# Optimization experiments

Hardware: AMD Instinct MI355X
Metric: run time of the kernel (lower is better)

## Reference

```python
import jax, jax.numpy as jnp
import numpy as np
from jax import lax

N, CIN, COUT, T, V, G, K = 32, 64, 64, 256, 25, 8, 3  # batch, channels, time, joints, groups, subsets
EPS = 1e-5  # BatchNorm eps


def setup_inputs() -> dict:
    key = jax.random.key(0)
    ks = jax.random.split(key, 10)
    x = jax.random.normal(ks[0], (N, CIN, T, V), jnp.float32)
    # DecoupleA param: A reshaped [3,1,V,V] tiled over groups (torch .repeat tiles)
    A0 = jax.random.uniform(ks[1], (K, 1, V, V), jnp.float32)
    DecoupleA = jnp.tile(A0, (1, G, 1, 1))
    W = jax.random.normal(ks[2], (CIN, COUT * K), jnp.float32) * np.float32(np.sqrt(0.5 / (COUT * K)))
    b = jnp.full((1, COUT * K, 1, 1), 1e-6, jnp.float32)
    g0 = 1.0 + 0.1 * jax.random.normal(ks[3], (COUT * K,), jnp.float32)
    b0 = 0.1 * jax.random.normal(ks[4], (COUT * K,), jnp.float32)
    g1 = 1.0 + 0.1 * jax.random.normal(ks[5], (COUT,), jnp.float32)
    b1 = 0.1 * jax.random.normal(ks[6], (COUT,), jnp.float32)
    conv_w = jax.random.normal(ks[7], (COUT, COUT, 9, 1), jnp.float32) * np.float32(np.sqrt(2.0 / (COUT * 9)))
    conv_b = jnp.zeros((COUT,), jnp.float32)
    g2 = 1.0 + 0.1 * jax.random.normal(ks[8], (COUT,), jnp.float32)
    b2 = 0.1 * jax.random.normal(ks[9], (COUT,), jnp.float32)
    return {"x": x, "DecoupleA": DecoupleA, "W": W, "b": b, "g0": g0, "b0": b0,
            "g1": g1, "b1": b1, "conv_w": conv_w, "conv_b": conv_b, "g2": g2, "b2": b2,
            "keep_prob": 1}


def _bn_eval(y, g, be):
    # inference BN with running_mean=0, running_var=1
    return y * (g / jnp.sqrt(1.0 + EPS))[None, :, None, None] + be[None, :, None, None]


def reference(x, DecoupleA, W, b, g0, b0, g1, b1, conv_w, conv_b, g2, b2, keep_prob):
    # ---- unit_gcn ----
    learn_A = jnp.tile(DecoupleA, (1, COUT // G, 1, 1))           # [3, COUT, V, V]
    # norm(): right-multiply by diag((colsum + 0.001)^-1) == scale columns
    invD = 1.0 / (jnp.sum(learn_A, axis=2) + 0.001)               # [3, COUT, V]
    normA = learn_A * invD[:, :, None, :]
    y = jnp.einsum('nctw,cd->ndtw', x, W) + b                     # [N, 3*COUT, T, V]
    y = _bn_eval(y, g0, b0)
    y = y.reshape(N, K, COUT, T, V)
    y = jnp.einsum('nkctv,kcvw->nctw', y, normA)                  # message passing
    y = _bn_eval(y, g1, b1)
    y = jax.nn.relu(y + x)                                        # down = identity (CIN==COUT)
    # ---- unit_tcn (keep_prob==1 -> DropBlocks are identity) ----
    z = lax.conv_general_dilated(y, conv_w, (1, 1), [(4, 4), (0, 0)],
                                 dimension_numbers=('NCHW', 'OIHW', 'NCHW'))
    z = z + conv_b[None, :, None, None]
    z = _bn_eval(z, g2, b2)
    # ---- residual (identity, CIN==COUT, stride=1; skip-DropBlocks identity) ----
    return jax.nn.relu(z + x)
```

## Files before the change

kernel.cpp:

```cpp
#include <hip/hip_runtime.h>
#include <hip/hip_bf16.h>
#include <stdint.h>


typedef const float* fp;
typedef __attribute__((ext_vector_type(8))) short short8;
typedef __attribute__((ext_vector_type(4))) float floatx4;

__device__ __forceinline__ float us2f(unsigned int u){
  union { unsigned int i; float f; } c; c.i = u << 16; return c.f;
}
__device__ __forceinline__ unsigned short f2us(float f){
  __hip_bfloat16 h = __float2bfloat16(f);
  return *reinterpret_cast<unsigned short*>(&h);
}
__device__ __forceinline__ void gload_lds16(const void* g, void* l){
  __builtin_amdgcn_global_load_lds(
      (const __attribute__((address_space(1))) void*)g,
      (__attribute__((address_space(3))) void*)l, 16, 0, 0);
}


__global__ __launch_bounds__(256) void k_pre(
    fp A, fp W, fp b, fp g0, fp b0, fp cw, fp cb, fp g2, fp b2,
    float* normA, float* Weff, float* beff, float* cbe, unsigned short* cwetb)
{
  int gid = blockIdx.x * 256 + threadIdx.x;
  const float inv_s = rsqrtf(1.0f + 1e-5f);

  if (gid < 16800) {
    int k  = gid / 5600;
    int r  = gid % 5600;
    int g  = r / 700;
    int r2 = r % 700;
    int v  = r2 / 28, w = r2 % 28;
    float val = 0.f;
    if (w < 25) {
      float s = 0.f;
      for (int vv = 0; vv < 25; vv++) s += A[((k*8+g)*25+vv)*25 + w];
      val = A[((k*8+g)*25+v)*25 + w] / (s + 0.001f);
    }
    normA[gid] = val;
    return;
  }
  gid -= 16800;
  if (gid < 12288) {
    int d = gid % 192;
    Weff[gid] = W[gid] * (g0[d] * inv_s);
    return;
  }
  gid -= 12288;
  if (gid < 192) {
    beff[gid] = b[gid] * (g0[gid] * inv_s) + b0[gid];
    return;
  }
  gid -= 192;
  if (gid < 64) {
    cbe[gid] = cb[gid] * (g2[gid] * inv_s) + b2[gid];
    return;
  }
  gid -= 64;
  if (gid < 36864) {
    int o = gid / 576, r = gid % 576;
    int j = r / 64, i = r % 64;
    cwetb[gid] = f2us(cw[(o*64+i)*9 + j] * (g2[o] * inv_s));
  }
}

__global__ __launch_bounds__(256) void k_pre2(
    const float* Weff, const float* beff, const float* normA, fp g1, fp b1,
    unsigned short* U, float* biasU)
{
  int m = blockIdx.x;
  int tid = threadIdx.x;
  if (m >= 1600) {
    for (int k = tid; k < 1600; k += 256) U[(long long)m*1600 + k] = 0;
    return;
  }
  int c = m & 63, w = m >> 6, g = c & 7;
  __shared__ float nAL[75];
  __shared__ float WeffL[192];
  if (tid < 75) {
    int kk = tid / 25, vv = tid % 25;
    nAL[tid] = normA[((kk*8 + g)*25 + vv)*28 + w];
  }
  if (tid < 192) {
    int kk = tid >> 6, cin = tid & 63;
    WeffL[tid] = Weff[cin*192 + kk*64 + c];
  }
  __syncthreads();
  float s1 = g1[c] * rsqrtf(1.0f + 1e-5f);
  for (int k = tid; k < 1600; k += 256) {
    int cin = k / 25, vv = k - cin*25;
    float acc = WeffL[cin]       * nAL[vv]
              + WeffL[64 + cin]  * nAL[25 + vv]
              + WeffL[128 + cin] * nAL[50 + vv];
    acc *= s1;
    if (cin == c && vv == w) acc += 1.0f;
    U[(long long)m*1600 + k] = f2us(acc);
  }
  if (tid == 0) {
    float acc = 0.f;
    for (int kk = 0; kk < 3; kk++) {
      float be = beff[kk*64 + c];
      for (int v = 0; v < 25; v++) acc += be * nAL[kk*25 + v];
    }
    biasU[m] = acc * s1 + b1[c];
  }
}

__global__ __launch_bounds__(256) void k_xt(fp x, unsigned short* xb)
{
  int n = blockIdx.x >> 5, tb = blockIdx.x & 31, t0 = tb*8, tid = threadIdx.x;
  __shared__ unsigned short xs[64*8*26];
  for (int e = tid; e < 12800; e += 256) {
    int c = e / 200, r = e - c*200, tt = r / 25, v = r - tt*25;
    xs[(c*8 + tt)*26 + v] = f2us(x[((n*64 + c)*256 + t0 + tt)*25 + v]);
  }
  __syncthreads();
  for (int e = tid; e < 12800; e += 256) {
    int tt = e / 1600, q = e - tt*1600, c = q / 25, v = q - c*25;
    xb[(n*256 + t0 + tt)*1600 + q] = xs[(c*8 + tt)*26 + v];
  }
}

__global__ __launch_bounds__(256, 2) void k_gemm(
    const unsigned short* U, const unsigned short* xb, const float* biasU,
    unsigned short* yb)
{
  int bm = blockIdx.x >> 6, bn = blockIdx.x & 63;
  int n = bn >> 1, t0 = (bn & 1) * 128;
  int tid = threadIdx.x, lane = tid & 63, wid = tid >> 6;
  int l15 = lane & 15, grp = lane >> 4;

  __shared__ __align__(16) unsigned short As[256*64];
  __shared__ __align__(16) unsigned short Bs[128*64];

  const unsigned short* gA[8];
  const unsigned short* gB[4];
  unsigned short* lA[8];
  unsigned short* lB[4];
  #pragma unroll
  for (int it = 0; it < 8; it++) {
    int e = it*256 + tid;
    int row = e >> 3, li = e & 7;
    int kcol = (li ^ (row & 7)) * 8;
    gA[it] = U + (long long)(bm*256 + row)*1600 + kcol;
    lA[it] = As + e*8;
  }
  #pragma unroll
  for (int it = 0; it < 4; it++) {
    int e = it*256 + tid;
    int row = e >> 3, li = e & 7;
    int kcol = (li ^ (row & 7)) * 8;
    gB[it] = xb + (long long)(n*256 + t0 + row)*1600 + kcol;
    lB[it] = Bs + e*8;
  }

  floatx4 acc[4][8];
  #pragma unroll
  for (int i = 0; i < 4; i++)
    #pragma unroll
    for (int j = 0; j < 8; j++) acc[i][j] = (floatx4){0.f,0.f,0.f,0.f};

  for (int kc = 0; kc < 25; kc++) {
    #pragma unroll
    for (int it = 0; it < 8; it++) gload_lds16(gA[it] + kc*64, lA[it]);
    #pragma unroll
    for (int it = 0; it < 4; it++) gload_lds16(gB[it] + kc*64, lB[it]);
    __syncthreads();
    #pragma unroll
    for (int ks = 0; ks < 2; ks++) {
      int colk = ((ks*4 + grp) ^ (l15 & 7)) * 8;
      short8 af[4], bf[8];
      #pragma unroll
      for (int i = 0; i < 4; i++)
        af[i] = *(const short8*)(As + (wid*64 + i*16 + l15)*64 + colk);
      #pragma unroll
      for (int j = 0; j < 8; j++)
        bf[j] = *(const short8*)(Bs + (j*16 + l15)*64 + colk);
      #pragma unroll
      for (int i = 0; i < 4; i++)
        #pragma unroll
        for (int j = 0; j < 8; j++)
          acc[i][j] = __builtin_amdgcn_mfma_f32_16x16x32_bf16(af[i], bf[j], acc[i][j], 0, 0, 0);
    }
    __syncthreads();
  }

  #pragma unroll
  for (int i = 0; i < 4; i++) {
    int mbase = bm*256 + wid*64 + i*16 + grp*4;
    if (mbase >= 1600) continue;
    float4 bu = *(const float4*)(biasU + mbase);
    #pragma unroll
    for (int j = 0; j < 8; j++) {
      int col = j*16 + l15;
      int t = t0 + col;
      ushort4 pk;
      pk.x = f2us(fmaxf(acc[i][j][0] + bu.x, 0.f));
      pk.y = f2us(fmaxf(acc[i][j][1] + bu.y, 0.f));
      pk.z = f2us(fmaxf(acc[i][j][2] + bu.z, 0.f));
      pk.w = f2us(fmaxf(acc[i][j][3] + bu.w, 0.f));
      *(ushort4*)(yb + (long long)(n*256 + t)*1600 + mbase) = pk;
    }
  }
}

__global__ __launch_bounds__(512) void k_tcn(
    const unsigned short* yb, const unsigned short* cwetb, const float* cbe,
    fp x, const unsigned short* zpg, float* out)
{
  int n = blockIdx.x >> 5, tb = blockIdx.x & 31, t0 = tb*8;
  int tid = threadIdx.x, lane = tid & 63, wid = tid >> 6;
  int l15 = lane & 15, grp = lane >> 4;
  __shared__ __align__(16) unsigned short ys[3584*8];

  #pragma unroll
  for (int it = 0; it < 7; it++) {
    int e = it*512 + tid;
    int row = e >> 3, li = e & 7;
    int rt = row / 25, v = row - rt*25;
    int tg = t0 - 4 + rt;
    int sli = li ^ (row & 7);
    bool ok = (row < 425) && (tg >= 0) && (tg < 256);
    const unsigned short* src = ok
      ? yb + ((long long)(n*256 + tg)*1600 + v*64 + sli*8)
      : zpg + li*8;
    gload_lds16(src, ys + e*8);
  }

  int p = wid & 3, h = wid >> 2;
  int o0 = p * 16;
  int o = o0 + l15;
  short8 af[9][2];
  #pragma unroll
  for (int j = 0; j < 9; j++) {
    af[j][0] = *(const short8*)(cwetb + ((o*9 + j)*64 + grp*8));
    af[j][1] = *(const short8*)(cwetb + ((o*9 + j)*64 + 32 + grp*8));
  }
  float4 cb4 = *(const float4*)(cbe + o0 + grp*4);
  __syncthreads();

  for (int tile = h; tile < 13; tile += 2) {
    int colb = tile*16 + l15;
    floatx4 acc = (floatx4){0.f,0.f,0.f,0.f};
    #pragma unroll
    for (int j = 0; j < 9; j++) {
      int row = colb + 25*j;
      int r7 = row & 7;
      const unsigned short* rb = ys + row*64;
      short8 b0 = *(const short8*)(rb + ((grp     ^ r7))*8);
      short8 b1 = *(const short8*)(rb + (((4+grp) ^ r7))*8);
      acc = __builtin_amdgcn_mfma_f32_16x16x32_bf16(af[j][0], b0, acc, 0, 0, 0);
      acc = __builtin_amdgcn_mfma_f32_16x16x32_bf16(af[j][1], b1, acc, 0, 0, 0);
    }
    if (colb < 200) {
      int tt = colb / 25, v = colb - tt*25, t = t0 + tt;
      #pragma unroll
      for (int r = 0; r < 4; r++) {
        int oo = o0 + grp*4 + r;
        float val = acc[r] + ((const float*)&cb4)[r]
                  + x[((n*64 + oo)*256 + t)*25 + v];
        out[((n*64 + oo)*256 + t)*25 + v] = fmaxf(val, 0.f);
      }
    }
  }
}

extern "C" void kernel_launch(void* const* d_in, const int* in_sizes, int n_in,
                              void* d_out, int out_size, void* d_ws, size_t ws_size,
                              hipStream_t stream)
{
  fp x  = (fp)d_in[0];
  fp A  = (fp)d_in[1];
  fp W  = (fp)d_in[2];
  fp b  = (fp)d_in[3];
  fp g0 = (fp)d_in[4];
  fp b0 = (fp)d_in[5];
  fp g1 = (fp)d_in[6];
  fp b1 = (fp)d_in[7];
  fp cw = (fp)d_in[8];
  fp cb = (fp)d_in[9];
  fp g2 = (fp)d_in[10];
  fp b2 = (fp)d_in[11];

  char* ws = (char*)d_ws;
  float*          normA = (float*)(ws + 0);
  float*          Weff  = (float*)(ws + 67584);
  float*          beff  = (float*)(ws + 116736);
  float*          cbe   = (float*)(ws + 117504);
  unsigned short* cwetb = (unsigned short*)(ws + 117760);
  float*          biasU = (float*)(ws + 191488);
  unsigned short* U     = (unsigned short*)(ws + 197888);
  unsigned short* xb    = (unsigned short*)(ws + 5932288);
  unsigned short* yb    = (unsigned short*)(ws + 32146688);
  const unsigned short* zpg = U + (long long)1600*1600;

  k_pre<<<259, 256, 0, stream>>>(A, W, b, g0, b0, cw, cb, g2, b2,
                                 normA, Weff, beff, cbe, cwetb);
  k_pre2<<<1792, 256, 0, stream>>>(Weff, beff, normA, g1, b1, U, biasU);
  k_xt<<<1024, 256, 0, stream>>>(x, xb);
  k_gemm<<<448, 256, 0, stream>>>(U, xb, biasU, yb);
  k_tcn<<<1024, 512, 0, stream>>>(yb, cwetb, cbe, x, zpg, (float*)d_out);
}
```

Before: 227.8 us.

## Rewrite GEMM as 256x256 double-buffered 8-wave pipeline with XCD block remap

The main GEMM kernel moves from a 256x128 single-buffered tile with 4 waves to a 256x256 tile with 8 waves. A and B tiles are double-buffered in LDS, with global-to-LDS loads for the next k-steps issued while MFMAs run on the current buffer. The inner loop is split into four phases separated by barriers and s_setprio, and the launch uses 224 blocks remapped across XCDs. This is meant to hide load latency and improve reuse, at the cost of 128KB of LDS per block, hand-placed waitcnt and barriers that are fragile, and fewer blocks than there are CUs.

```diff
diff --git a/kernel.cpp b/kernel.cpp
--- a/kernel.cpp
+++ b/kernel.cpp
@@ -19,6 +19,9 @@
       (const __attribute__((address_space(1))) void*)g,
       (__attribute__((address_space(3))) void*)l, 16, 0, 0);
 }
+
+#define BARRIER() asm volatile("s_barrier" ::: "memory")
+#define VMCNT(n)  asm volatile("s_waitcnt vmcnt(" #n ")" ::: "memory")
 
 
 __global__ __launch_bounds__(256) void k_pre(
@@ -124,85 +127,160 @@
   }
 }
 
-__global__ __launch_bounds__(256, 2) void k_gemm(
+__global__ __launch_bounds__(512, 2) void k_gemm(
     const unsigned short* U, const unsigned short* xb, const float* biasU,
     unsigned short* yb)
 {
-  int bm = blockIdx.x >> 6, bn = blockIdx.x & 63;
-  int n = bn >> 1, t0 = (bn & 1) * 128;
+  int bid = blockIdx.x;
+  int lb  = (bid & 7) * 28 + (bid >> 3);
+  int bm = lb >> 5, bn = lb & 31;
   int tid = threadIdx.x, lane = tid & 63, wid = tid >> 6;
   int l15 = lane & 15, grp = lane >> 4;
-
-  __shared__ __align__(16) unsigned short As[256*64];
-  __shared__ __align__(16) unsigned short Bs[128*64];
-
-  const unsigned short* gA[8];
-  const unsigned short* gB[4];
-  unsigned short* lA[8];
-  unsigned short* lB[4];
-  #pragma unroll
-  for (int it = 0; it < 8; it++) {
-    int e = it*256 + tid;
-    int row = e >> 3, li = e & 7;
-    int kcol = (li ^ (row & 7)) * 8;
-    gA[it] = U + (long long)(bm*256 + row)*1600 + kcol;
-    lA[it] = As + e*8;
-  }
-  #pragma unroll
-  for (int it = 0; it < 4; it++) {
-    int e = it*256 + tid;
-    int row = e >> 3, li = e & 7;
-    int kcol = (li ^ (row & 7)) * 8;
-    gB[it] = xb + (long long)(n*256 + t0 + row)*1600 + kcol;
-    lB[it] = Bs + e*8;
-  }
-
-  floatx4 acc[4][8];
-  #pragma unroll
-  for (int i = 0; i < 4; i++)
-    #pragma unroll
-    for (int j = 0; j < 8; j++) acc[i][j] = (floatx4){0.f,0.f,0.f,0.f};
-
-  for (int kc = 0; kc < 25; kc++) {
-    #pragma unroll
-    for (int it = 0; it < 8; it++) gload_lds16(gA[it] + kc*64, lA[it]);
-    #pragma unroll
-    for (int it = 0; it < 4; it++) gload_lds16(gB[it] + kc*64, lB[it]);
-    __syncthreads();
-    #pragma unroll
-    for (int ks = 0; ks < 2; ks++) {
-      int colk = ((ks*4 + grp) ^ (l15 & 7)) * 8;
-      short8 af[4], bf[8];
-      #pragma unroll
-      for (int i = 0; i < 4; i++)
-        af[i] = *(const short8*)(As + (wid*64 + i*16 + l15)*64 + colk);
-      #pragma unroll
-      for (int j = 0; j < 8; j++)
-        bf[j] = *(const short8*)(Bs + (j*16 + l15)*64 + colk);
+  int wm = wid >> 2, wn = wid & 3;
+
+  __shared__ __align__(16) unsigned short AsB[2][16384];
+  __shared__ __align__(16) unsigned short BsB[2][16384];
+
+  int srow = tid >> 3, sli = tid & 7;
+  int sgrp = sli ^ (srow & 7);
+  const unsigned short* gA = U  + (long long)(bm*256 + srow)*1600 + sgrp*8;
+  const unsigned short* gB = xb + (long long)(bn*256 + srow)*1600 + sgrp*8;
+
+  auto stA = [&](int kt, int slot, int it){
+    gload_lds16(gA + (long long)it*102400 + kt*64, &AsB[slot][(it*512 + tid)*8]);
+  };
+  auto stB = [&](int kt, int slot, int it){
+    gload_lds16(gB + (long long)it*102400 + kt*64, &BsB[slot][(it*512 + tid)*8]);
+  };
+
+  int arow = wm*128 + l15;
+  int brow = wn*64  + l15;
+  int swz  = l15 & 7;
+  auto rdA = [&](int slot, int i, int ks) -> short8 {
+    return *(const short8*)(&AsB[slot][(arow + i*16)*64 + (((ks*4 + grp) ^ swz))*8]);
+  };
+  auto rdB = [&](int slot, int j, int ks) -> short8 {
+    return *(const short8*)(&BsB[slot][(brow + j*16)*64 + (((ks*4 + grp) ^ swz))*8]);
+  };
+
+  floatx4 acc[8][4];
+  #pragma unroll
+  for (int i = 0; i < 8; i++)
+    #pragma unroll
+    for (int j = 0; j < 4; j++) acc[i][j] = (floatx4){0.f,0.f,0.f,0.f};
+
+  #pragma unroll
+  for (int it = 0; it < 4; it++) stA(0, 0, it);
+  #pragma unroll
+  for (int it = 0; it < 4; it++) stB(0, 0, it);
+  #pragma unroll
+  for (int it = 0; it < 4; it++) stA(1, 1, it);
+  VMCNT(4);
+  BARRIER();
+
+  for (int kt = 0; kt < 25; ++kt) {
+    int cs = kt & 1, ns = cs ^ 1;
+
+    short8 aR[2][4], bR[2][2];
+    #pragma unroll
+    for (int ks = 0; ks < 2; ks++)
+      #pragma unroll
+      for (int i = 0; i < 4; i++) aR[ks][i] = rdA(cs, i, ks);
+    #pragma unroll
+    for (int ks = 0; ks < 2; ks++)
+      #pragma unroll
+      for (int j = 0; j < 2; j++) bR[ks][j] = rdB(cs, j, ks);
+    if (kt + 1 < 25) { stB(kt+1, ns, 0); stB(kt+1, ns, 1); }
+    BARRIER();
+    __builtin_amdgcn_sched_barrier(0);
+    __builtin_amdgcn_s_setprio(1);
+    #pragma unroll
+    for (int ks = 0; ks < 2; ks++)
       #pragma unroll
       for (int i = 0; i < 4; i++)
         #pragma unroll
-        for (int j = 0; j < 8; j++)
-          acc[i][j] = __builtin_amdgcn_mfma_f32_16x16x32_bf16(af[i], bf[j], acc[i][j], 0, 0, 0);
-    }
-    __syncthreads();
-  }
-
-  #pragma unroll
-  for (int i = 0; i < 4; i++) {
-    int mbase = bm*256 + wid*64 + i*16 + grp*4;
-    if (mbase >= 1600) continue;
-    float4 bu = *(const float4*)(biasU + mbase);
-    #pragma unroll
-    for (int j = 0; j < 8; j++) {
-      int col = j*16 + l15;
-      int t = t0 + col;
+        for (int j = 0; j < 2; j++)
+          acc[i][j] = __builtin_amdgcn_mfma_f32_16x16x32_bf16(aR[ks][i], bR[ks][j], acc[i][j], 0, 0, 0);
+    __builtin_amdgcn_s_setprio(0);
+    BARRIER();
+
+    short8 bR2[2][2];
+    #pragma unroll
+    for (int ks = 0; ks < 2; ks++)
+      #pragma unroll
+      for (int j = 0; j < 2; j++) bR2[ks][j] = rdB(cs, 2 + j, ks);
+    if (kt + 1 < 25) { stB(kt+1, ns, 2); stB(kt+1, ns, 3); }
+    BARRIER();
+    __builtin_amdgcn_sched_barrier(0);
+    __builtin_amdgcn_s_setprio(1);
+    #pragma unroll
+    for (int ks = 0; ks < 2; ks++)
+      #pragma unroll
+      for (int i = 0; i < 4; i++)
+        #pragma unroll
+        for (int j = 0; j < 2; j++)
+          acc[i][2+j] = __builtin_amdgcn_mfma_f32_16x16x32_bf16(aR[ks][i], bR2[ks][j], acc[i][2+j], 0, 0, 0);
+    __builtin_amdgcn_s_setprio(0);
+    BARRIER();
+
+    short8 aR2[2][4];
+    #pragma unroll
+    for (int ks = 0; ks < 2; ks++)
+      #pragma unroll
+      for (int i = 0; i < 4; i++) aR2[ks][i] = rdA(cs, 4 + i, ks);
+    BARRIER();
+    __builtin_amdgcn_sched_barrier(0);
+    __builtin_amdgcn_s_setprio(1);
+    #pragma unroll
+    for (int ks = 0; ks < 2; ks++)
+      #pragma unroll
+      for (int i = 0; i < 4; i++)
+        #pragma unroll
+        for (int j = 0; j < 2; j++)
+          acc[4+i][2+j] = __builtin_amdgcn_mfma_f32_16x16x32_bf16(aR2[ks][i], bR2[ks][j], acc[4+i][2+j], 0, 0, 0);
+    __builtin_amdgcn_s_setprio(0);
+    BARRIER();
+
+    short8 bR3[2][2];
+    #pragma unroll
+    for (int ks = 0; ks < 2; ks++)
+      #pragma unroll
+      for (int j = 0; j < 2; j++) bR3[ks][j] = rdB(cs, j, ks);
+    if (kt + 2 < 25) {
+      #pragma unroll
+      for (int it = 0; it < 4; it++) stA(kt+2, cs, it);
+      VMCNT(4);
+    } else if (kt == 23) {
+      VMCNT(0);
+    }
+    BARRIER();
+    __builtin_amdgcn_sched_barrier(0);
+    __builtin_amdgcn_s_setprio(1);
+    #pragma unroll
+    for (int ks = 0; ks < 2; ks++)
+      #pragma unroll
+      for (int i = 0; i < 4; i++)
+        #pragma unroll
+        for (int j = 0; j < 2; j++)
+          acc[4+i][j] = __builtin_amdgcn_mfma_f32_16x16x32_bf16(aR2[ks][i], bR3[ks][j], acc[4+i][j], 0, 0, 0);
+    __builtin_amdgcn_s_setprio(0);
+    BARRIER();
+  }
+
+  #pragma unroll
+  for (int i = 0; i < 8; i++) {
+    int mb = bm*256 + wm*128 + i*16 + grp*4;
+    if (mb >= 1600) continue;
+    float4 bu = *(const float4*)(biasU + mb);
+    #pragma unroll
+    for (int j = 0; j < 4; j++) {
+      int nrow = bn*256 + wn*64 + j*16 + l15;
       ushort4 pk;
       pk.x = f2us(fmaxf(acc[i][j][0] + bu.x, 0.f));
       pk.y = f2us(fmaxf(acc[i][j][1] + bu.y, 0.f));
       pk.z = f2us(fmaxf(acc[i][j][2] + bu.z, 0.f));
       pk.w = f2us(fmaxf(acc[i][j][3] + bu.w, 0.f));
-      *(ushort4*)(yb + (long long)(n*256 + t)*1600 + mbase) = pk;
+      *(ushort4*)(yb + (long long)nrow*1600 + mb) = pk;
     }
   }
 }
@@ -301,6 +379,6 @@
                                  normA, Weff, beff, cbe, cwetb);
   k_pre2<<<1792, 256, 0, stream>>>(Weff, beff, normA, g1, b1, U, biasU);
   k_xt<<<1024, 256, 0, stream>>>(x, xb);
-  k_gemm<<<448, 256, 0, stream>>>(U, xb, biasU, yb);
+  k_gemm<<<224, 512, 0, stream>>>(U, xb, biasU, yb);
   k_tcn<<<1024, 512, 0, stream>>>(yb, cwetb, cbe, x, zpg, (float*)d_out);
 }
```

Result: slower. 246.3 us (+8.1%).
